# Performance work log

Measured on AMD Instinct MI355X. Metric: run time of the kernel, lower is better.

The kernel has to match this reference:

```python
import jax, jax.numpy as jnp
import numpy as np

EMBED_DIM = 1024
NUM_HEADS = 16
HEAD_DIM = EMBED_DIM // NUM_HEADS
SCALE = HEAD_DIM ** -0.5


def setup_inputs() -> dict:
    key = jax.random.key(0)
    k_x, k_wqkv, k_bqkv, k_wp, k_bp = jax.random.split(key, 5)
    B, N = 2, 2048
    x = jax.random.normal(k_x, (B, N, EMBED_DIM), dtype=jnp.float32)
    # torch.nn.Linear default init: U(-1/sqrt(fan_in), 1/sqrt(fan_in))
    lim = 1.0 / np.sqrt(EMBED_DIM)
    W_qkv = jax.random.uniform(k_wqkv, (EMBED_DIM, 3 * EMBED_DIM), jnp.float32, -lim, lim)
    b_qkv = jax.random.uniform(k_bqkv, (3 * EMBED_DIM,), jnp.float32, -lim, lim)
    W_proj = jax.random.uniform(k_wp, (EMBED_DIM, EMBED_DIM), jnp.float32, -lim, lim)
    b_proj = jax.random.uniform(k_bp, (EMBED_DIM,), jnp.float32, -lim, lim)
    return {"x": x, "W_qkv": W_qkv, "b_qkv": b_qkv, "W_proj": W_proj, "b_proj": b_proj}


def reference(x, W_qkv, b_qkv, W_proj, b_proj):
    B, N, C = x.shape
    qkv = x @ W_qkv + b_qkv                              # [B, N, 3C]
    qkv = qkv.reshape(B, N, 3, NUM_HEADS, HEAD_DIM)
    qkv = jnp.transpose(qkv, (2, 0, 3, 1, 4))            # [3, B, H, N, D]
    q, k, v = qkv[0], qkv[1], qkv[2]
    attn = jnp.einsum('bhnd,bhmd->bhnm', q, k) * SCALE   # [B, H, N, N]
    attn = jax.nn.softmax(attn, axis=-1)
    out = jnp.einsum('bhnm,bhmd->bhnd', attn, v)         # [B, H, N, D]
    out = jnp.transpose(out, (0, 2, 1, 3)).reshape(B, N, C)
    return out @ W_proj + b_proj
```

## Files before the change

kernel.cpp:

```cpp
#include <hip/hip_runtime.h>
#include <math.h>

typedef unsigned short u16;
typedef _Float16 f16;
typedef f16 f16x8 __attribute__((ext_vector_type(8)));
typedef __fp16 hp16x2 __attribute__((ext_vector_type(2)));
typedef float f32x4 __attribute__((ext_vector_type(4)));
typedef float f32x16 __attribute__((ext_vector_type(16)));

#define SEQ   2048
#define NH    16
#define HD    64
#define EMB   1024
#define NQKV  3072
#define BATCH 2
#define PSTR  72
#define QSCALE 0.18033688f

__device__ __forceinline__ u16 f2h(float f) {
  union { f16 h; u16 u; } w; w.h = (f16)f; return w.u;
}

__device__ __forceinline__ void gload16(const void* g, void* l) {
  __builtin_amdgcn_global_load_lds(
      (const __attribute__((address_space(1))) unsigned int*)g,
      (__attribute__((address_space(3))) unsigned int*)l, 16, 0, 0);
}

__global__ __launch_bounds__(256) void cvt_x(const float* __restrict__ X,
                                             u16* __restrict__ Xh) {
  const size_t i = ((size_t)blockIdx.x * 256 + threadIdx.x) * 8;
  float4 a = *reinterpret_cast<const float4*>(&X[i]);
  float4 b = *reinterpret_cast<const float4*>(&X[i + 4]);
  union { hp16x2 h2[4]; float4 f; } pk;
  pk.h2[0] = __builtin_amdgcn_cvt_pkrtz(a.x, a.y);
  pk.h2[1] = __builtin_amdgcn_cvt_pkrtz(a.z, a.w);
  pk.h2[2] = __builtin_amdgcn_cvt_pkrtz(b.x, b.y);
  pk.h2[3] = __builtin_amdgcn_cvt_pkrtz(b.z, b.w);
  *reinterpret_cast<float4*>(&Xh[i]) = pk.f;
}

__global__ __launch_bounds__(256) void cvt_wt(const float* __restrict__ W,
                                              u16* __restrict__ Wt,
                                              int K, int N) {
  __shared__ u16 T[64][68];
  const int n0 = blockIdx.x << 6, k0 = blockIdx.y << 6;
  const int t = threadIdx.x;
  const int rr = t >> 4, cc = (t & 15) << 2;
#pragma unroll
  for (int p = 0; p < 4; p++) {
    const int kr = p * 16 + rr;
    float4 v = *reinterpret_cast<const float4*>(&W[(size_t)(k0 + kr) * N + n0 + cc]);
    T[cc + 0][kr] = f2h(v.x); T[cc + 1][kr] = f2h(v.y);
    T[cc + 2][kr] = f2h(v.z); T[cc + 3][kr] = f2h(v.w);
  }
  __syncthreads();
#pragma unroll
  for (int p = 0; p < 4; p++) {
    const int nr = p * 16 + rr;
    union { u16 s[4]; unsigned long long d; } o;
    o.s[0] = T[nr][cc + 0]; o.s[1] = T[nr][cc + 1];
    o.s[2] = T[nr][cc + 2]; o.s[3] = T[nr][cc + 3];
    *reinterpret_cast<unsigned long long*>(&Wt[(size_t)(n0 + nr) * K + k0 + cc]) = o.d;
  }
}

__device__ __forceinline__ void gemm_core(const u16* __restrict__ Ag,
                                          const u16* __restrict__ Bg,
                                          int m0, int n0, int t,
                                          f32x4 acc[4][4]) {
  __shared__ __align__(16) u16 As[128 * 32];
  __shared__ __align__(16) u16 Bs[128 * 32];
  const int lane = t & 63, w = t >> 6;
  const int l15  = lane & 15, quad = lane >> 4;
  const int wm = w >> 1, wn = w & 1;
  const int srow  = lane >> 2;
  const int gslot = (lane & 3) ^ ((srow >> 1) & 3);
  const int xk    = (quad ^ ((l15 >> 1) & 3)) << 3;

  for (int k0 = 0; k0 < EMB; k0 += 32) {
    __syncthreads();
#pragma unroll
    for (int i = 0; i < 2; i++) {
      const int ca = w * 2 + i;
      const int arow = ca * 16 + srow;
      gload16(Ag + (size_t)(m0 + arow) * EMB + k0 + gslot * 8, &As[ca * 512]);
      gload16(Bg + (size_t)(n0 + arow) * EMB + k0 + gslot * 8, &Bs[ca * 512]);
    }
    __syncthreads();
    f16x8 af[4], bf[4];
#pragma unroll
    for (int s = 0; s < 4; s++)
      af[s] = *reinterpret_cast<const f16x8*>(&As[(wm * 64 + s * 16 + l15) * 32 + xk]);
#pragma unroll
    for (int s = 0; s < 4; s++)
      bf[s] = *reinterpret_cast<const f16x8*>(&Bs[(wn * 64 + s * 16 + l15) * 32 + xk]);
#pragma unroll
    for (int i = 0; i < 4; i++)
#pragma unroll
      for (int j = 0; j < 4; j++)
        acc[i][j] = __builtin_amdgcn_mfma_f32_16x16x32_f16(af[i], bf[j], acc[i][j], 0, 0, 0);
  }
}

__global__ __launch_bounds__(256) void k_qkv(const u16* __restrict__ Ag,
                                             const u16* __restrict__ Bg,
                                             const float* __restrict__ bias,
                                             u16* __restrict__ qo,
                                             u16* __restrict__ ko,
                                             u16* __restrict__ vo) {
  const int t = threadIdx.x;
  const int lane = t & 63, w = t >> 6;
  const int l15 = lane & 15, quad = lane >> 4;
  const int wm = w >> 1, wn = w & 1;
  const int m0 = blockIdx.y << 7, n0 = blockIdx.x << 7;
  f32x4 acc[4][4];
#pragma unroll
  for (int i = 0; i < 4; i++)
#pragma unroll
    for (int j = 0; j < 4; j++) acc[i][j] = (f32x4){0.f, 0.f, 0.f, 0.f};
  gemm_core(Ag, Bg, m0, n0, t, acc);
#pragma unroll
  for (int j = 0; j < 4; j++) {
    const int c = n0 + wn * 64 + j * 16 + l15;
    const int which = c >> 10, h = (c >> 6) & 15, d = c & 63;
    const float bv = bias[c];
    const float sc = (which == 0) ? QSCALE : 1.0f;
#pragma unroll
    for (int i = 0; i < 4; i++) {
#pragma unroll
      for (int r = 0; r < 4; r++) {
        const int m  = m0 + wm * 64 + i * 16 + quad * 4 + r;
        const int bb = m >> 11, n = m & (SEQ - 1);
        const u16 val = f2h((acc[i][j][r] + bv) * sc);
        if (which == 2)
          vo[(((size_t)bb * NH + h) * HD + d) * SEQ + n] = val;
        else if (which == 1)
          ko[((((size_t)bb * NH + h) * SEQ) + n) * HD + d] = val;
        else
          qo[((((size_t)bb * NH + h) * SEQ) + n) * HD + d] = val;
      }
    }
  }
}

__global__ __launch_bounds__(256) void k_proj(const u16* __restrict__ Ag,
                                              const u16* __restrict__ Bg,
                                              const float* __restrict__ bias,
                                              float* __restrict__ out) {
  const int t = threadIdx.x;
  const int lane = t & 63, w = t >> 6;
  const int l15 = lane & 15, quad = lane >> 4;
  const int wm = w >> 1, wn = w & 1;
  const int m0 = blockIdx.y << 7, n0 = blockIdx.x << 7;
  f32x4 acc[4][4];
#pragma unroll
  for (int i = 0; i < 4; i++)
#pragma unroll
    for (int j = 0; j < 4; j++) acc[i][j] = (f32x4){0.f, 0.f, 0.f, 0.f};
  gemm_core(Ag, Bg, m0, n0, t, acc);
#pragma unroll
  for (int j = 0; j < 4; j++) {
    const int c = n0 + wn * 64 + j * 16 + l15;
    const float bv = bias[c];
#pragma unroll
    for (int i = 0; i < 4; i++) {
#pragma unroll
      for (int r = 0; r < 4; r++) {
        const int m = m0 + wm * 64 + i * 16 + quad * 4 + r;
        out[(size_t)m * EMB + c] = acc[i][j][r] + bv;
      }
    }
  }
}

__global__ __launch_bounds__(256) void k_attn(const u16* __restrict__ Qg,
                                              const u16* __restrict__ Kg,
                                              const u16* __restrict__ Vtg,
                                              u16* __restrict__ AO) {
  __shared__ __align__(16) u16 Ks[64 * 64];
  __shared__ __align__(16) u16 Vs[64 * 64];
  __shared__ __align__(16) u16 Ps[4 * 32 * PSTR];
  const int t    = threadIdx.x;
  const int lane = t & 63, w = t >> 6;
  const int l31  = lane & 31, hi = lane >> 5;
  const int bh   = blockIdx.y;
  const int q0   = blockIdx.x << 7;
  const size_t base = (size_t)bh * SEQ * HD;

  f16x8 qf[4];
  {
    const u16* qp = Qg + base + (size_t)(q0 + 32 * w + l31) * HD + hi * 8;
#pragma unroll
    for (int c = 0; c < 4; c++) {
      union { float4 f; f16x8 v; } fu;
      fu.f = *reinterpret_cast<const float4*>(qp + c * 16);
      qf[c] = fu.v;
    }
  }

  f32x16 O0 = {}, O1 = {};
  float lsum = 0.f;
  const int fsw = (l31 >> 1) & 7;
  const int srw = lane >> 3, ssl = lane & 7;
  u16* Pw = &Ps[w * 32 * PSTR];

  for (int kt = 0; kt < SEQ; kt += 64) {
    __syncthreads();
#pragma unroll
    for (int i = 0; i < 2; i++) {
      const int ca  = w * 2 + i;
      const int row = ca * 8 + srw;
      const int sg  = (ssl ^ ((row >> 1) & 7)) << 3;
      gload16(Kg  + base + (size_t)(kt + row) * HD + sg, &Ks[ca * 512]);
      gload16(Vtg + base + (size_t)row * SEQ + kt + sg,  &Vs[ca * 512]);
    }
    __syncthreads();

#pragma unroll
    for (int sk = 0; sk < 2; sk++) {
      f32x16 c = {};
#pragma unroll
      for (int cc = 0; cc < 4; cc++) {
        f16x8 kf = *reinterpret_cast<const f16x8*>(
            &Ks[(sk * 32 + l31) * 64 + (((cc * 2 + hi) ^ fsw) << 3)]);
        c = __builtin_amdgcn_mfma_f32_32x32x16_f16(kf, qf[cc], c, 0, 0, 0);
      }
#pragma unroll
      for (int g = 0; g < 4; g++) {
        const float p0 = exp2f(c[4 * g + 0]);
        const float p1 = exp2f(c[4 * g + 1]);
        const float p2 = exp2f(c[4 * g + 2]);
        const float p3 = exp2f(c[4 * g + 3]);
        lsum += (p0 + p1) + (p2 + p3);
        union { hp16x2 h2[2]; unsigned long long d; } pk;
        pk.h2[0] = __builtin_amdgcn_cvt_pkrtz(p0, p1);
        pk.h2[1] = __builtin_amdgcn_cvt_pkrtz(p2, p3);
        *reinterpret_cast<unsigned long long*>(
            &Pw[l31 * PSTR + sk * 32 + g * 8 + 4 * hi]) = pk.d;
      }
    }

#pragma unroll
    for (int cc = 0; cc < 4; cc++) {
      f16x8 pf = *reinterpret_cast<const f16x8*>(&Pw[l31 * PSTR + cc * 16 + hi * 8]);
      f16x8 vf0 = *reinterpret_cast<const f16x8*>(
          &Vs[l31 * 64 + (((cc * 2 + hi) ^ fsw) << 3)]);
      f16x8 vf1 = *reinterpret_cast<const f16x8*>(
          &Vs[(32 + l31) * 64 + (((cc * 2 + hi) ^ fsw) << 3)]);
      O0 = __builtin_amdgcn_mfma_f32_32x32x16_f16(pf, vf0, O0, 0, 0, 0);
      O1 = __builtin_amdgcn_mfma_f32_32x32x16_f16(pf, vf1, O1, 0, 0, 0);
    }
  }

  lsum += __shfl_xor(lsum, 32);
  const int b = bh >> 4, h = bh & 15;
#pragma unroll
  for (int g = 0; g < 4; g++) {
#pragma unroll
    for (int rr = 0; rr < 4; rr++) {
      const int r = g * 4 + rr;
      const int qrow = rr + 8 * g + 4 * hi;
      const float inv = 1.f / __shfl(lsum, qrow, 64);
      const int n = q0 + 32 * w + qrow;
      u16* dst = AO + ((size_t)(b * SEQ + n)) * EMB + h * HD;
      dst[l31]      = f2h(O0[r] * inv);
      dst[32 + l31] = f2h(O1[r] * inv);
    }
  }
}

extern "C" void kernel_launch(void* const* d_in, const int* in_sizes, int n_in,
                              void* d_out, int out_size, void* d_ws, size_t ws_size,
                              hipStream_t stream) {
  (void)in_sizes; (void)n_in; (void)out_size; (void)ws_size;
  const float* x     = (const float*)d_in[0];
  const float* Wqkv  = (const float*)d_in[1];
  const float* bqkv  = (const float*)d_in[2];
  const float* Wproj = (const float*)d_in[3];
  const float* bproj = (const float*)d_in[4];
  float* out = (float*)d_out;

  const size_t NE = (size_t)BATCH * SEQ * EMB;
  u16* q    = (u16*)d_ws;
  u16* k    = q + NE;
  u16* vt   = k + NE;
  u16* aoxh = vt + NE;
  u16* Wt   = aoxh + NE;
  u16* Wpt  = Wt + (size_t)NQKV * EMB;

  cvt_x<<<NE / 2048, 256, 0, stream>>>(x, aoxh);
  dim3 gw1(NQKV / 64, EMB / 64);
  cvt_wt<<<gw1, 256, 0, stream>>>(Wqkv, Wt, EMB, NQKV);
  dim3 gw2(EMB / 64, EMB / 64);
  cvt_wt<<<gw2, 256, 0, stream>>>(Wproj, Wpt, EMB, EMB);

  dim3 gq(NQKV / 128, (BATCH * SEQ) / 128);
  k_qkv<<<gq, 256, 0, stream>>>(aoxh, Wt, bqkv, q, k, vt);

  dim3 ga(SEQ / 128, BATCH * NH);
  k_attn<<<ga, 256, 0, stream>>>(q, k, vt, aoxh);

  dim3 gp(EMB / 128, (BATCH * SEQ) / 128);
  k_proj<<<gp, 256, 0, stream>>>(aoxh, Wpt, bproj, out);
}
```

Before: 218.2 us.

## Double-buffer K/V tiles and keep softmax probabilities in registers via lane shuffles

The attention kernel now double-buffers the K and V^T tiles in LDS. It issues the async global-to-LDS load for the next tile right after a single barrier, so loads overlap compute, and drops the second barrier per iteration. The P matrix is no longer written to and re-read from shared memory. It is rearranged into MFMA A-operand layout with packed fp16 conversions and cross-half-wave shuffles. Blocks shrink to 2 waves covering 64 query rows, doubling the grid, which raises block count but halves K/V reuse per staged tile.

```diff
diff --git a/kernel.cpp b/kernel.cpp
--- a/kernel.cpp
+++ b/kernel.cpp
@@ -2,6 +2,7 @@
 #include <math.h>
 
 typedef unsigned short u16;
+typedef unsigned int u32;
 typedef _Float16 f16;
 typedef f16 f16x8 __attribute__((ext_vector_type(8)));
 typedef __fp16 hp16x2 __attribute__((ext_vector_type(2)));
@@ -14,11 +15,13 @@
 #define EMB   1024
 #define NQKV  3072
 #define BATCH 2
-#define PSTR  72
 #define QSCALE 0.18033688f
 
 __device__ __forceinline__ u16 f2h(float f) {
   union { f16 h; u16 u; } w; w.h = (f16)f; return w.u;
+}
+__device__ __forceinline__ u32 pk2(float a, float b) {
+  union { hp16x2 h; u32 u; } w; w.h = __builtin_amdgcn_cvt_pkrtz(a, b); return w.u;
 }
 
 __device__ __forceinline__ void gload16(const void* g, void* l) {
@@ -32,11 +35,9 @@
   const size_t i = ((size_t)blockIdx.x * 256 + threadIdx.x) * 8;
   float4 a = *reinterpret_cast<const float4*>(&X[i]);
   float4 b = *reinterpret_cast<const float4*>(&X[i + 4]);
-  union { hp16x2 h2[4]; float4 f; } pk;
-  pk.h2[0] = __builtin_amdgcn_cvt_pkrtz(a.x, a.y);
-  pk.h2[1] = __builtin_amdgcn_cvt_pkrtz(a.z, a.w);
-  pk.h2[2] = __builtin_amdgcn_cvt_pkrtz(b.x, b.y);
-  pk.h2[3] = __builtin_amdgcn_cvt_pkrtz(b.z, b.w);
+  union { u32 u[4]; float4 f; } pk;
+  pk.u[0] = pk2(a.x, a.y); pk.u[1] = pk2(a.z, a.w);
+  pk.u[2] = pk2(b.x, b.y); pk.u[3] = pk2(b.z, b.w);
   *reinterpret_cast<float4*>(&Xh[i]) = pk.f;
 }
 
@@ -174,18 +175,17 @@
   }
 }
 
-__global__ __launch_bounds__(256) void k_attn(const u16* __restrict__ Qg,
+__global__ __launch_bounds__(128) void k_attn(const u16* __restrict__ Qg,
                                               const u16* __restrict__ Kg,
                                               const u16* __restrict__ Vtg,
                                               u16* __restrict__ AO) {
-  __shared__ __align__(16) u16 Ks[64 * 64];
-  __shared__ __align__(16) u16 Vs[64 * 64];
-  __shared__ __align__(16) u16 Ps[4 * 32 * PSTR];
+  __shared__ __align__(16) u16 Ks[2][64 * 64];
+  __shared__ __align__(16) u16 Vs[2][64 * 64];
   const int t    = threadIdx.x;
   const int lane = t & 63, w = t >> 6;
   const int l31  = lane & 31, hi = lane >> 5;
   const int bh   = blockIdx.y;
-  const int q0   = blockIdx.x << 7;
+  const int q0   = blockIdx.x << 6;
   const size_t base = (size_t)bh * SEQ * HD;
 
   f16x8 qf[4];
@@ -203,54 +203,72 @@
   float lsum = 0.f;
   const int fsw = (l31 >> 1) & 7;
   const int srw = lane >> 3, ssl = lane & 7;
-  u16* Pw = &Ps[w * 32 * PSTR];
-
+
+  auto stage = [&](int buf, int kt) {
+#pragma unroll
+    for (int i = 0; i < 4; i++) {
+      const int ca  = w * 4 + i;
+      const int row = ca * 8 + srw;
+      const int sg  = (ssl ^ ((row >> 1) & 7)) << 3;
+      gload16(Kg  + base + (size_t)(kt + row) * HD + sg, &Ks[buf][ca * 512]);
+      gload16(Vtg + base + (size_t)row * SEQ + kt + sg,  &Vs[buf][ca * 512]);
+    }
+  };
+
+  stage(0, 0);
+  int cur = 0;
   for (int kt = 0; kt < SEQ; kt += 64) {
     __syncthreads();
-#pragma unroll
-    for (int i = 0; i < 2; i++) {
-      const int ca  = w * 2 + i;
-      const int row = ca * 8 + srw;
-      const int sg  = (ssl ^ ((row >> 1) & 7)) << 3;
-      gload16(Kg  + base + (size_t)(kt + row) * HD + sg, &Ks[ca * 512]);
-      gload16(Vtg + base + (size_t)row * SEQ + kt + sg,  &Vs[ca * 512]);
-    }
-    __syncthreads();
-
+    if (kt + 64 < SEQ) stage(cur ^ 1, kt + 64);
+    const u16* Kb = Ks[cur];
+    const u16* Vb = Vs[cur];
+
+    f16x8 pA[4];
 #pragma unroll
     for (int sk = 0; sk < 2; sk++) {
       f32x16 c = {};
 #pragma unroll
       for (int cc = 0; cc < 4; cc++) {
         f16x8 kf = *reinterpret_cast<const f16x8*>(
-            &Ks[(sk * 32 + l31) * 64 + (((cc * 2 + hi) ^ fsw) << 3)]);
+            &Kb[(sk * 32 + l31) * 64 + (((cc * 2 + hi) ^ fsw) << 3)]);
         c = __builtin_amdgcn_mfma_f32_32x32x16_f16(kf, qf[cc], c, 0, 0, 0);
       }
-#pragma unroll
-      for (int g = 0; g < 4; g++) {
-        const float p0 = exp2f(c[4 * g + 0]);
-        const float p1 = exp2f(c[4 * g + 1]);
-        const float p2 = exp2f(c[4 * g + 2]);
-        const float p3 = exp2f(c[4 * g + 3]);
-        lsum += (p0 + p1) + (p2 + p3);
-        union { hp16x2 h2[2]; unsigned long long d; } pk;
-        pk.h2[0] = __builtin_amdgcn_cvt_pkrtz(p0, p1);
-        pk.h2[1] = __builtin_amdgcn_cvt_pkrtz(p2, p3);
-        *reinterpret_cast<unsigned long long*>(
-            &Pw[l31 * PSTR + sk * 32 + g * 8 + 4 * hi]) = pk.d;
-      }
-    }
-
-#pragma unroll
-    for (int cc = 0; cc < 4; cc++) {
-      f16x8 pf = *reinterpret_cast<const f16x8*>(&Pw[l31 * PSTR + cc * 16 + hi * 8]);
+      float p[16];
+#pragma unroll
+      for (int r = 0; r < 16; r++) {
+        p[r] = exp2f(c[r]);
+        lsum += p[r];
+      }
+#pragma unroll
+      for (int wd = 0; wd < 2; wd++) {
+        const float* pg = &p[wd * 8];
+        const u32 A = pk2(pg[0], pg[1]);
+        const u32 B = pk2(pg[2], pg[3]);
+        const u32 C = pk2(pg[4], pg[5]);
+        const u32 D = pk2(pg[6], pg[7]);
+        const u32 x = hi ? A : C;
+        const u32 y = hi ? B : D;
+        const u32 sx = __shfl_xor(x, 32);
+        const u32 sy = __shfl_xor(y, 32);
+        union { u32 u[4]; f16x8 v; } fr;
+        fr.u[0] = hi ? sx : A;
+        fr.u[1] = hi ? sy : B;
+        fr.u[2] = hi ? C : sx;
+        fr.u[3] = hi ? D : sy;
+        pA[sk * 2 + wd] = fr.v;
+      }
+    }
+
+#pragma unroll
+    for (int win = 0; win < 4; win++) {
       f16x8 vf0 = *reinterpret_cast<const f16x8*>(
-          &Vs[l31 * 64 + (((cc * 2 + hi) ^ fsw) << 3)]);
+          &Vb[l31 * 64 + (((win * 2 + hi) ^ fsw) << 3)]);
       f16x8 vf1 = *reinterpret_cast<const f16x8*>(
-          &Vs[(32 + l31) * 64 + (((cc * 2 + hi) ^ fsw) << 3)]);
-      O0 = __builtin_amdgcn_mfma_f32_32x32x16_f16(pf, vf0, O0, 0, 0, 0);
-      O1 = __builtin_amdgcn_mfma_f32_32x32x16_f16(pf, vf1, O1, 0, 0, 0);
-    }
+          &Vb[(32 + l31) * 64 + (((win * 2 + hi) ^ fsw) << 3)]);
+      O0 = __builtin_amdgcn_mfma_f32_32x32x16_f16(pA[win], vf0, O0, 0, 0, 0);
+      O1 = __builtin_amdgcn_mfma_f32_32x32x16_f16(pA[win], vf1, O1, 0, 0, 0);
+    }
+    cur ^= 1;
   }
 
   lsum += __shfl_xor(lsum, 32);
@@ -298,8 +316,8 @@
   dim3 gq(NQKV / 128, (BATCH * SEQ) / 128);
   k_qkv<<<gq, 256, 0, stream>>>(aoxh, Wt, bqkv, q, k, vt);
 
-  dim3 ga(SEQ / 128, BATCH * NH);
-  k_attn<<<ga, 256, 0, stream>>>(q, k, vt, aoxh);
+  dim3 ga(SEQ / 64, BATCH * NH);
+  k_attn<<<ga, 128, 0, stream>>>(q, k, vt, aoxh);
 
   dim3 gp(EMB / 128, (BATCH * SEQ) / 128);
   k_proj<<<gp, 256, 0, stream>>>(aoxh, Wpt, bproj, out);
```

Result: slower. 230.9 us (+5.8%).
